# Kernel tuning notes

Hardware: AMD Instinct MI355X
Metric: run time of the kernel (lower is better)

## Reference

```python
import jax, jax.numpy as jnp
import numpy as np

SCALE = 1.0  # noise std from __init__


def setup_inputs() -> dict:
    key = jax.random.key(0)
    k1, k2, k3 = jax.random.split(key, 3)
    B, N, D, T = 32, 1024, 64, 2048
    data = jax.random.normal(k1, (B, N, D), dtype=jnp.float32)
    targets = jax.random.normal(k2, (B, N), dtype=jnp.float32)
    # W = task_pool.squeeze(-1).T, shape (n_dims, n_tasks)
    W = jax.random.normal(k3, (D, T), dtype=jnp.float32)
    return {"data": data, "targets": targets, "W": W}


def reference(data, targets, W):
    # data: (B, N, D), targets: (B, N), W: (D, T)
    dtype = data.dtype
    log_scale_sq = 2.0 * jnp.log(jnp.asarray(SCALE, dtype))
    # per-point per-task Gaussian log-likelihood terms
    XW = jnp.einsum('bnd,dt->bnt', data, W)                 # (B, N, T)
    diff = targets[..., None] - XW
    log_probs = -0.5 * ((diff / SCALE) ** 2 + log_scale_sq)  # (B, N, T)
    # exclusive prefix-sum over points: posterior at point i uses points < i.
    # At i=0 alpha=0 -> uniform weights -> W.mean(axis=1), matching the
    # original's explicit w_mean first step.
    cum = jnp.cumsum(log_probs, axis=1)
    alpha = jnp.concatenate([jnp.zeros_like(cum[:, :1]), cum[:, :-1]], axis=1)
    weights = jax.nn.softmax(alpha, axis=-1)                 # (B, N, T)
    w_mmse = jnp.einsum('bnt,dt->bnd', weights, W)           # (B, N, D)
    preds = jnp.einsum('bnd,bnd->bn', data, w_mmse)          # (B, N)
    return preds
```

## Files before the change

kernel.cpp:

```cpp
#include <hip/hip_runtime.h>
#include <hip/hip_bf16.h>
#include <math.h>

#define BB 32
#define NN 1024
#define DD 64
#define TT 2048
#define CHUNKS (TT / 256)
#define SEGS 16

typedef float f32x4 __attribute__((ext_vector_type(4)));
typedef unsigned short u16x4 __attribute__((ext_vector_type(4)));
using s16x8 = __attribute__((ext_vector_type(8))) short;

#define NLOG2E_HALF (-0.72134752044448169f)

__device__ __forceinline__ float exp2_fast(float x) {
    return __builtin_amdgcn_exp2f(x);
}

template<int CTRL>
__device__ __forceinline__ float dpp_mov_f(float v) {
    return __int_as_float(
        __builtin_amdgcn_mov_dpp(__float_as_int(v), CTRL, 0xF, 0xF, true));
}

template<int GB>
__device__ __forceinline__ float groupMax(float v) {
    v = fmaxf(v, dpp_mov_f<0x0B1>(v));
    v = fmaxf(v, dpp_mov_f<0x04E>(v));
    v = fmaxf(v, dpp_mov_f<0x141>(v));
    v = fmaxf(v, dpp_mov_f<0x140>(v));
    if constexpr (GB >= 5) v = fmaxf(v, __shfl_xor(v, 16));
    if constexpr (GB >= 6) v = fmaxf(v, __shfl_xor(v, 32));
    return v;
}

template<int GB>
__device__ __forceinline__ float groupSum(float v) {
    v += dpp_mov_f<0x0B1>(v);
    v += dpp_mov_f<0x04E>(v);
    v += dpp_mov_f<0x141>(v);
    v += dpp_mov_f<0x140>(v);
    if constexpr (GB >= 5) v += __shfl_xor(v, 16);
    if constexpr (GB >= 6) v += __shfl_xor(v, 32);
    return v;
}

__device__ __forceinline__ unsigned short bf16_rne(float x) {
    unsigned u = __float_as_uint(x);
    return (unsigned short)((u + 0x7FFFu + ((u >> 16) & 1u)) >> 16);
}
__device__ __forceinline__ void bf16_split(float x, unsigned short& hi,
                                           unsigned short& lo) {
    const unsigned short h = bf16_rne(x);
    const float xh = __uint_as_float(((unsigned)h) << 16);
    hi = h;
    lo = bf16_rne(x - xh);
}

__device__ __forceinline__ void loadW(const float* __restrict__ W, int col,
                                      f32x4* wv) {
#pragma unroll
    for (int i = 0; i < 16; ++i) {
        wv[i].x = W[(size_t)(4 * i + 0) * TT + col];
        wv[i].y = W[(size_t)(4 * i + 1) * TT + col];
        wv[i].z = W[(size_t)(4 * i + 2) * TT + col];
        wv[i].w = W[(size_t)(4 * i + 3) * TT + col];
    }
}

__device__ __forceinline__ float hsum(f32x4 s) {
    return (s.x + s.y) + (s.z + s.w);
}

__device__ __forceinline__ void dot4(const float* __restrict__ x0p,
                                     const f32x4* wv, float* xw) {
    const f32x4* xr0 = (const f32x4*)(x0p);
    const f32x4* xr1 = (const f32x4*)(x0p + DD);
    const f32x4* xr2 = (const f32x4*)(x0p + 2 * DD);
    const f32x4* xr3 = (const f32x4*)(x0p + 3 * DD);
    f32x4 s0 = {0.f, 0.f, 0.f, 0.f};
    f32x4 s1 = {0.f, 0.f, 0.f, 0.f};
    f32x4 s2 = {0.f, 0.f, 0.f, 0.f};
    f32x4 s3 = {0.f, 0.f, 0.f, 0.f};
#pragma unroll
    for (int i = 0; i < 16; ++i) {
        const f32x4 w = wv[i];
        s0 += xr0[i] * w;
        s1 += xr1[i] * w;
        s2 += xr2[i] * w;
        s3 += xr3[i] * w;
    }
    xw[0] = hsum(s0); xw[1] = hsum(s1); xw[2] = hsum(s2); xw[3] = hsum(s3);
}


__global__ __launch_bounds__(256)
void xsplit_kernel(const float* __restrict__ x,
                   unsigned short* __restrict__ xh,
                   unsigned short* __restrict__ xl)
{
    const int idx = (blockIdx.x * 256 + threadIdx.x) * 4;
    const f32x4 v = *(const f32x4*)(x + idx);
    u16x4 h, lo;
#pragma unroll
    for (int j = 0; j < 4; ++j) {
        unsigned short hh, ll;
        bf16_split(v[j], hh, ll);
        h[j] = hh; lo[j] = ll;
    }
    *(u16x4*)(xh + idx) = h;
    *(u16x4*)(xl + idx) = lo;
}

__global__ __launch_bounds__(256)
void wsplitT_kernel(const float* __restrict__ W,
                    unsigned short* __restrict__ whT,
                    unsigned short* __restrict__ wlT)
{
    const int idx = blockIdx.x * 256 + threadIdx.x;
    const int t = idx & (TT - 1);
    const int d = idx >> 11;
    unsigned short h, lo;
    bf16_split(W[(size_t)d * TT + t], h, lo);
    whT[(size_t)t * DD + d] = h;
    wlT[(size_t)t * DD + d] = lo;
}


__device__ __forceinline__ void loadB64_pre(const unsigned short* __restrict__ whT,
                                            const unsigned short* __restrict__ wlT,
                                            int colbase, int l,
                                            s16x8 bh[2][4], s16x8 bl[2][4]) {
    const int c0 = colbase + (l & 15);
    const int kb = (l >> 4) * 8;
#pragma unroll
    for (int ks = 0; ks < 2; ++ks)
#pragma unroll
        for (int nt = 0; nt < 4; ++nt) {
            const size_t off = (size_t)(c0 + nt * 16) * DD + ks * 32 + kb;
            bh[ks][nt] = *(const s16x8*)(whT + off);
            bl[ks][nt] = *(const s16x8*)(wlT + off);
        }
}

__device__ __forceinline__ void mfma_tile16_pre(const unsigned short* __restrict__ xh,
                                                const unsigned short* __restrict__ xl,
                                                int tile_n0, int l,
                                                const s16x8 bh[2][4],
                                                const s16x8 bl[2][4],
                                                f32x4 acc[4]) {
#pragma unroll
    for (int nt = 0; nt < 4; ++nt) acc[nt] = (f32x4){0.f, 0.f, 0.f, 0.f};
    const int row = tile_n0 + (l & 15);
#pragma unroll
    for (int ks = 0; ks < 2; ++ks) {
        const size_t off = (size_t)row * DD + ks * 32 + (l >> 4) * 8;
        const s16x8 ah = *(const s16x8*)(xh + off);
        const s16x8 al = *(const s16x8*)(xl + off);
#pragma unroll
        for (int nt = 0; nt < 4; ++nt) {
            acc[nt] = __builtin_amdgcn_mfma_f32_16x16x32_bf16(ah, bh[ks][nt], acc[nt], 0, 0, 0);
            acc[nt] = __builtin_amdgcn_mfma_f32_16x16x32_bf16(ah, bl[ks][nt], acc[nt], 0, 0, 0);
            acc[nt] = __builtin_amdgcn_mfma_f32_16x16x32_bf16(al, bh[ks][nt], acc[nt], 0, 0, 0);
        }
    }
}

template<int SEG>
__global__ __launch_bounds__(256)
void segsum_mfma_kernel(const unsigned short* __restrict__ xh,
                        const unsigned short* __restrict__ xl,
                        const unsigned short* __restrict__ whT,
                        const unsigned short* __restrict__ wlT,
                        const float* __restrict__ targets,
                        float* __restrict__ segsum)
{
    constexpr int NSEG = NN / SEG;
    __shared__ float ts[NSEG];

    const int blk   = blockIdx.x;
    const int s     = blk % SEG;
    const int rem   = blk / SEG;
    const int chunk = rem % CHUNKS;
    const int b     = rem / CHUNKS;
    const int tid   = threadIdx.x;
    const int wv    = tid >> 6;
    const int l     = tid & 63;

    const unsigned short* xbh = xh + (size_t)b * NN * DD;
    const unsigned short* xbl = xl + (size_t)b * NN * DD;
    const float* tb = targets + (size_t)b * NN;
    const int n0 = s * NSEG;

    if (tid < NSEG) ts[tid] = tb[n0 + tid];

    s16x8 bh[2][4], bl[2][4];
    loadB64_pre(whT, wlT, chunk * 256 + wv * 64, l, bh, bl);
    __syncthreads();

    float colacc[4] = {0.f, 0.f, 0.f, 0.f};

#pragma unroll 1
    for (int h = 0; h < NSEG / 16; ++h) {
        f32x4 acc[4];
        mfma_tile16_pre(xbh, xbl, n0 + h * 16, l, bh, bl, acc);
#pragma unroll
        for (int r = 0; r < 4; ++r) {
            const float tv = ts[h * 16 + (l >> 4) * 4 + r];
#pragma unroll
            for (int nt = 0; nt < 4; ++nt) {
                const float d = tv - acc[nt][r];
                colacc[nt] = fmaf(d * d, NLOG2E_HALF, colacc[nt]);
            }
        }
    }

#pragma unroll
    for (int nt = 0; nt < 4; ++nt) {
        colacc[nt] += __shfl_xor(colacc[nt], 16);
        colacc[nt] += __shfl_xor(colacc[nt], 32);
    }

    if (l < 16) {
        const size_t base = ((size_t)b * SEG + s) * TT + chunk * 256 + wv * 64 + l;
#pragma unroll
        for (int nt = 0; nt < 4; ++nt) segsum[base + nt * 16] = colacc[nt];
    }
}

template<int SEG, int GB>
__global__ __launch_bounds__(64)
void scan_mfma1_kernel(const unsigned short* __restrict__ xh,
                       const unsigned short* __restrict__ xl,
                       const unsigned short* __restrict__ whT,
                       const unsigned short* __restrict__ wlT,
                       const float* __restrict__ targets,
                       const float* __restrict__ segsum,
                       float* __restrict__ mP,
                       float* __restrict__ sP,
                       float* __restrict__ pP)
{
    constexpr int NSEG = NN / SEG;
    constexpr int MT   = 16;
    constexpr int CG   = TT / 64;
    constexpr int PPN  = TT >> GB;

    __shared__ __align__(16) float xw_tile[MT][68];

    const int blk = blockIdx.x;
    const int s   = blk % SEG;
    const int rem = blk / SEG;
    const int cg  = rem % CG;
    const int b   = rem / CG;
    const int l   = threadIdx.x;
    const int col = cg * 64 + l;

    const unsigned short* xbh = xh + (size_t)b * NN * DD;
    const unsigned short* xbl = xl + (size_t)b * NN * DD;
    const float* tb = targets + (size_t)b * NN;

    s16x8 bh[2][4], bl[2][4];
    loadB64_pre(whT, wlT, cg * 64, l, bh, bl);

    const int  k16    = col >> GB;
    const bool writer = (l & ((1 << GB) - 1)) == 0;
    const size_t base0 = (size_t)b * NN * PPN + k16;

    float alpha = 0.0f;
    if constexpr (SEG > 1) {
        for (int s2 = 0; s2 < s; ++s2)
            alpha += segsum[((size_t)b * SEG + s2) * TT + col];
    }

    const int n0 = s * NSEG;

#pragma unroll 1
    for (int h = 0; h < NSEG / MT; ++h) {
        f32x4 acc[4];
        mfma_tile16_pre(xbh, xbl, n0 + h * MT, l, bh, bl, acc);

#pragma unroll
        for (int nt = 0; nt < 4; ++nt)
#pragma unroll
            for (int r = 0; r < 4; ++r)
                xw_tile[(l >> 4) * 4 + r][nt * 16 + (l & 15)] = acc[nt][r];

#pragma unroll 1
        for (int q = 0; q < MT; q += 4) {
            const int n = n0 + h * MT + q;
            float xw[4];
#pragma unroll
            for (int j = 0; j < 4; ++j) xw[j] = xw_tile[q + j][l];

            float a[4];
            float al_ = alpha;
#pragma unroll
            for (int j = 0; j < 4; ++j) {
                a[j] = al_;
                const float d = tb[n + j] - xw[j];
                al_ = fmaf(d * d, NLOG2E_HALF, al_);
            }
            alpha = al_;

            float m[4], e[4], qv[4], sv[4], pv[4];
#pragma unroll
            for (int j = 0; j < 4; ++j) m[j] = groupMax<GB>(a[j]);
#pragma unroll
            for (int j = 0; j < 4; ++j) {
                e[j]  = exp2_fast(a[j] - m[j]);
                qv[j] = e[j] * xw[j];
            }
#pragma unroll
            for (int j = 0; j < 4; ++j) sv[j] = groupSum<GB>(e[j]);
#pragma unroll
            for (int j = 0; j < 4; ++j) pv[j] = groupSum<GB>(qv[j]);

            if (writer) {
                const size_t i0 = base0 + (size_t)n * PPN;
#pragma unroll
                for (int j = 0; j < 4; ++j) {
                    mP[i0 + (size_t)j * PPN] = m[j];
                    sP[i0 + (size_t)j * PPN] = sv[j];
                    pP[i0 + (size_t)j * PPN] = pv[j];
                }
            }
        }
    }
}

template<int SEG, int GB>
__global__ __launch_bounds__(256, 4)
void scan_kernel(const float* __restrict__ data,
                 const float* __restrict__ targets,
                 const float* __restrict__ W,
                 const float* __restrict__ segsum,
                 float* __restrict__ mP,
                 float* __restrict__ sP,
                 float* __restrict__ pP)
{
    constexpr int NSEG = NN / SEG;
    constexpr int PPN  = TT >> GB;
    const int blk   = blockIdx.x;
    const int s     = blk % SEG;
    const int rem   = blk / SEG;
    const int chunk = rem % CHUNKS;
    const int b     = rem / CHUNKS;
    const int tid   = threadIdx.x;
    const int lane  = tid & 63;
    const int col   = chunk * 256 + tid;

    f32x4 wv[16];
    loadW(W, col, wv);

    const float* xb = data + (size_t)b * NN * DD;
    const float* tb = targets + (size_t)b * NN;

    const int  k      = (chunk * 256 + (tid & ~((1 << GB) - 1))) >> GB;
    const bool writer = (lane & ((1 << GB) - 1)) == 0;
    const size_t base0 = (size_t)b * NN * PPN + k;

    float alpha = 0.0f;
    if constexpr (SEG > 1) {
        for (int s2 = 0; s2 < s; ++s2)
            alpha += segsum[((size_t)b * SEG + s2) * TT + col];
    }

    const int n0 = s * NSEG;
    for (int n = n0; n < n0 + NSEG; n += 4) {
        float xw[4];
        dot4(xb + (size_t)n * DD, wv, xw);
        float a[4];
        float al = alpha;
#pragma unroll
        for (int j = 0; j < 4; ++j) {
            a[j] = al;
            const float d = tb[n + j] - xw[j];
            al = fmaf(d * d, NLOG2E_HALF, al);
        }
        alpha = al;
        float m[4], e[4], qv[4], sv[4], pv[4];
#pragma unroll
        for (int j = 0; j < 4; ++j) m[j] = groupMax<GB>(a[j]);
#pragma unroll
        for (int j = 0; j < 4; ++j) {
            e[j]  = exp2_fast(a[j] - m[j]);
            qv[j] = e[j] * xw[j];
        }
#pragma unroll
        for (int j = 0; j < 4; ++j) sv[j] = groupSum<GB>(e[j]);
#pragma unroll
        for (int j = 0; j < 4; ++j) pv[j] = groupSum<GB>(qv[j]);
        if (writer) {
            const size_t i0 = base0 + (size_t)n * PPN;
#pragma unroll
            for (int j = 0; j < 4; ++j) {
                mP[i0 + (size_t)j * PPN] = m[j];
                sP[i0 + (size_t)j * PPN] = sv[j];
                pP[i0 + (size_t)j * PPN] = pv[j];
            }
        }
    }
}

template<int PPN>
__global__ __launch_bounds__(256)
void combine_kernel(const float* __restrict__ mP,
                    const float* __restrict__ sP,
                    const float* __restrict__ pP,
                    float* __restrict__ out)
{
    const int wgid = blockIdx.x * 4 + (threadIdx.x >> 6);
    const int lane = threadIdx.x & 63;
    const size_t base = (size_t)wgid * PPN;

    float m = -INFINITY, s = 0.0f, p = 0.0f;
    if constexpr (PPN >= 64) {
#pragma unroll
        for (int j = 0; j < PPN / 64; ++j) {
            const size_t idx = base + lane + j * 64;
            const float mk = mP[idx], sk = sP[idx], pk = pP[idx];
            const float M  = fmaxf(m, mk);
            const float e1 = exp2_fast(m - M), e2 = exp2_fast(mk - M);
            s = s * e1 + sk * e2;
            p = p * e1 + pk * e2;
            m = M;
        }
    } else {
        if (lane < PPN) {
            m = mP[base + lane]; s = sP[base + lane]; p = pP[base + lane];
        }
    }

#pragma unroll
    for (int off = 1; off < 64; off <<= 1) {
        const float mo = __shfl_xor(m, off);
        const float so = __shfl_xor(s, off);
        const float po = __shfl_xor(p, off);
        const float M  = fmaxf(m, mo);
        const float e1 = exp2_fast(m - M), e2 = exp2_fast(mo - M);
        s = s * e1 + so * e2;
        p = p * e1 + po * e2;
        m = M;
    }

    if (lane == 0) out[wgid] = p / s;
}

extern "C" void kernel_launch(void* const* d_in, const int* in_sizes, int n_in,
                              void* d_out, int out_size, void* d_ws, size_t ws_size,
                              hipStream_t stream)
{
    (void)in_sizes; (void)n_in; (void)out_size;
    const float* data    = (const float*)d_in[0];
    const float* targets = (const float*)d_in[1];
    const float* W       = (const float*)d_in[2];
    float* out = (float*)d_out;

    const size_t plane4 = (size_t)BB * NN * (TT >> 4);
    const size_t plane5 = (size_t)BB * NN * (TT >> 5);
    const size_t plane6 = (size_t)BB * NN * (TT >> 6);
    const size_t seg16  = (size_t)BB * SEGS * TT;
    const size_t xsplitF = (size_t)BB * NN * DD / 2;
    const size_t wsplitF = (size_t)TT * DD / 2;

    const int seg_grid  = BB * SEGS * CHUNKS;
    const int scan_grid = BB * (TT / 64) * SEGS;

    auto launch_pre = [&](size_t plane, auto scanTag) {
        float* mP = (float*)d_ws;
        float* sP = mP + plane;
        float* pP = sP + plane;
        float* sg = pP + plane;
        unsigned short* xh  = (unsigned short*)(sg + seg16);
        unsigned short* xl  = xh + (size_t)BB * NN * DD;
        unsigned short* whT = xl + (size_t)BB * NN * DD;
        unsigned short* wlT = whT + (size_t)TT * DD;

        xsplit_kernel<<<(BB * NN * DD) / (256 * 4), 256, 0, stream>>>(data, xh, xl);
        wsplitT_kernel<<<(TT * DD) / 256, 256, 0, stream>>>(W, whT, wlT);
        segsum_mfma_kernel<SEGS><<<seg_grid, 256, 0, stream>>>(xh, xl, whT, wlT, targets, sg);
        constexpr int GBv = decltype(scanTag)::value;
        scan_mfma1_kernel<SEGS, GBv><<<scan_grid, 64, 0, stream>>>(xh, xl, whT, wlT, targets, sg, mP, sP, pP);
        combine_kernel<(TT >> GBv)><<<(BB * NN) / 4, 256, 0, stream>>>(mP, sP, pP, out);
    };

    const size_t need4 = (3 * plane4 + seg16 + 2 * xsplitF + 2 * wsplitF) * sizeof(float);
    const size_t need5 = (3 * plane5 + seg16 + 2 * xsplitF + 2 * wsplitF) * sizeof(float);
    const size_t need6 = (3 * plane6 + seg16 + 2 * xsplitF + 2 * wsplitF) * sizeof(float);

    if (ws_size >= need4) {
        launch_pre(plane4, std::integral_constant<int, 4>{});
    } else if (ws_size >= need5) {
        launch_pre(plane5, std::integral_constant<int, 5>{});
    } else if (ws_size >= need6) {
        launch_pre(plane6, std::integral_constant<int, 6>{});
    } else {
        float* mP = (float*)d_ws;
        float* sP = mP + plane6;
        float* pP = sP + plane6;
        scan_kernel<1, 6><<<BB * CHUNKS, 256, 0, stream>>>(data, targets, W, nullptr, mP, sP, pP);
        combine_kernel<32><<<(BB * NN) / 4, 256, 0, stream>>>(mP, sP, pP, out);
    }
}
```

Baseline: 180.9 us.

## Merge split kernels into one launch and pack four scan waves per block

The separate x and W bf16-split kernels become a single launch whose blocks branch on block index, saving one kernel launch. The scan kernel moves from 64-thread blocks to 256-thread blocks, with four wavefronts each covering a different 64-column group and each using its own shared-memory tile slice. The intent is to reduce launch overhead and per-block scheduling cost and to improve occupancy packing. In exchange, each block needs four times the LDS, and the grid has a quarter as many blocks, which may change how work is balanced across CUs.

```diff
diff --git a/kernel.cpp b/kernel.cpp
--- a/kernel.cpp
+++ b/kernel.cpp
@@ -95,37 +95,38 @@
     xw[0] = hsum(s0); xw[1] = hsum(s1); xw[2] = hsum(s2); xw[3] = hsum(s3);
 }
 
-
+#define XB ((BB * NN * DD) / (256 * 4))
+#define WB ((TT * DD) / 256)
 __global__ __launch_bounds__(256)
-void xsplit_kernel(const float* __restrict__ x,
-                   unsigned short* __restrict__ xh,
-                   unsigned short* __restrict__ xl)
+void split_kernel(const float* __restrict__ x,
+                  const float* __restrict__ W,
+                  unsigned short* __restrict__ xh,
+                  unsigned short* __restrict__ xl,
+                  unsigned short* __restrict__ whT,
+                  unsigned short* __restrict__ wlT)
 {
-    const int idx = (blockIdx.x * 256 + threadIdx.x) * 4;
-    const f32x4 v = *(const f32x4*)(x + idx);
-    u16x4 h, lo;
-#pragma unroll
-    for (int j = 0; j < 4; ++j) {
-        unsigned short hh, ll;
-        bf16_split(v[j], hh, ll);
-        h[j] = hh; lo[j] = ll;
-    }
-    *(u16x4*)(xh + idx) = h;
-    *(u16x4*)(xl + idx) = lo;
-}
-
-__global__ __launch_bounds__(256)
-void wsplitT_kernel(const float* __restrict__ W,
-                    unsigned short* __restrict__ whT,
-                    unsigned short* __restrict__ wlT)
-{
-    const int idx = blockIdx.x * 256 + threadIdx.x;
-    const int t = idx & (TT - 1);
-    const int d = idx >> 11;
-    unsigned short h, lo;
-    bf16_split(W[(size_t)d * TT + t], h, lo);
-    whT[(size_t)t * DD + d] = h;
-    wlT[(size_t)t * DD + d] = lo;
+    const int gid = blockIdx.x;
+    if (gid < XB) {
+        const int idx = (gid * 256 + threadIdx.x) * 4;
+        const f32x4 v = *(const f32x4*)(x + idx);
+        u16x4 h, lo;
+#pragma unroll
+        for (int j = 0; j < 4; ++j) {
+            unsigned short hh, ll;
+            bf16_split(v[j], hh, ll);
+            h[j] = hh; lo[j] = ll;
+        }
+        *(u16x4*)(xh + idx) = h;
+        *(u16x4*)(xl + idx) = lo;
+    } else {
+        const int idx = (gid - XB) * 256 + threadIdx.x;
+        const int t = idx & (TT - 1);
+        const int d = idx >> 11;
+        unsigned short h, lo;
+        bf16_split(W[(size_t)d * TT + t], h, lo);
+        whT[(size_t)t * DD + d] = h;
+        wlT[(size_t)t * DD + d] = lo;
+    }
 }
 
 
@@ -231,8 +232,8 @@
 }
 
 template<int SEG, int GB>
-__global__ __launch_bounds__(64)
-void scan_mfma1_kernel(const unsigned short* __restrict__ xh,
+__global__ __launch_bounds__(256)
+void scan_mfma4_kernel(const unsigned short* __restrict__ xh,
                        const unsigned short* __restrict__ xl,
                        const unsigned short* __restrict__ whT,
                        const unsigned short* __restrict__ wlT,
@@ -244,17 +245,20 @@
 {
     constexpr int NSEG = NN / SEG;
     constexpr int MT   = 16;
-    constexpr int CG   = TT / 64;
+    constexpr int CGQ  = TT / 256;
     constexpr int PPN  = TT >> GB;
 
-    __shared__ __align__(16) float xw_tile[MT][68];
+    __shared__ __align__(16) float xw_tile[4][MT][68];
 
     const int blk = blockIdx.x;
     const int s   = blk % SEG;
     const int rem = blk / SEG;
-    const int cg  = rem % CG;
-    const int b   = rem / CG;
-    const int l   = threadIdx.x;
+    const int cgq = rem % CGQ;
+    const int b   = rem / CGQ;
+    const int tid = threadIdx.x;
+    const int wv  = tid >> 6;
+    const int l   = tid & 63;
+    const int cg  = cgq * 4 + wv;
     const int col = cg * 64 + l;
 
     const unsigned short* xbh = xh + (size_t)b * NN * DD;
@@ -285,14 +289,14 @@
         for (int nt = 0; nt < 4; ++nt)
 #pragma unroll
             for (int r = 0; r < 4; ++r)
-                xw_tile[(l >> 4) * 4 + r][nt * 16 + (l & 15)] = acc[nt][r];
+                xw_tile[wv][(l >> 4) * 4 + r][nt * 16 + (l & 15)] = acc[nt][r];
 
 #pragma unroll 1
         for (int q = 0; q < MT; q += 4) {
             const int n = n0 + h * MT + q;
             float xw[4];
 #pragma unroll
-            for (int j = 0; j < 4; ++j) xw[j] = xw_tile[q + j][l];
+            for (int j = 0; j < 4; ++j) xw[j] = xw_tile[wv][q + j][l];
 
             float a[4];
             float al_ = alpha;
@@ -466,9 +470,9 @@
     const size_t wsplitF = (size_t)TT * DD / 2;
 
     const int seg_grid  = BB * SEGS * CHUNKS;
-    const int scan_grid = BB * (TT / 64) * SEGS;
-
-    auto launch_pre = [&](size_t plane, auto scanTag) {
+    const int scan_grid = BB * (TT / 256) * SEGS;
+
+    auto launch_pre = [&](size_t plane, auto gbTag) {
         float* mP = (float*)d_ws;
         float* sP = mP + plane;
         float* pP = sP + plane;
@@ -478,11 +482,10 @@
         unsigned short* whT = xl + (size_t)BB * NN * DD;
         unsigned short* wlT = whT + (size_t)TT * DD;
 
-        xsplit_kernel<<<(BB * NN * DD) / (256 * 4), 256, 0, stream>>>(data, xh, xl);
-        wsplitT_kernel<<<(TT * DD) / 256, 256, 0, stream>>>(W, whT, wlT);
+        split_kernel<<<XB + WB, 256, 0, stream>>>(data, W, xh, xl, whT, wlT);
         segsum_mfma_kernel<SEGS><<<seg_grid, 256, 0, stream>>>(xh, xl, whT, wlT, targets, sg);
-        constexpr int GBv = decltype(scanTag)::value;
-        scan_mfma1_kernel<SEGS, GBv><<<scan_grid, 64, 0, stream>>>(xh, xl, whT, wlT, targets, sg, mP, sP, pP);
+        constexpr int GBv = decltype(gbTag)::value;
+        scan_mfma4_kernel<SEGS, GBv><<<scan_grid, 256, 0, stream>>>(xh, xl, whT, wlT, targets, sg, mP, sP, pP);
         combine_kernel<(TT >> GBv)><<<(BB * NN) / 4, 256, 0, stream>>>(mP, sP, pP, out);
     };
 
```

Measured after the change: 182.0 us. No clear change (+0.6%).

## Fuse bf16 split into segsum kernel and pair two segments per scan block

Applied to the files above, without the earlier changes.

Removes the separate x and W bf16 hi/lo split kernels: the segment-sum kernel now reads fp32 data and W directly, splits them in registers, and writes the split copies from designated blocks for the later scan kernel. The scan kernel now processes two segments per 64-thread block, interleaving the MFMA tile for the second segment with the softmax of the first to hide latency, which halves the grid. This cuts two launches and a full pass over the data, but adds redundant fp32 loads and split arithmetic in the segsum kernel. It also relies on the scan kernel seeing split data written by other blocks of the previous launch.

```diff
diff --git a/kernel.cpp b/kernel.cpp
--- a/kernel.cpp
+++ b/kernel.cpp
@@ -10,7 +10,6 @@
 #define SEGS 16
 
 typedef float f32x4 __attribute__((ext_vector_type(4)));
-typedef unsigned short u16x4 __attribute__((ext_vector_type(4)));
 using s16x8 = __attribute__((ext_vector_type(8))) short;
 
 #define NLOG2E_HALF (-0.72134752044448169f)
@@ -96,36 +95,67 @@
 }
 
 
-__global__ __launch_bounds__(256)
-void xsplit_kernel(const float* __restrict__ x,
-                   unsigned short* __restrict__ xh,
-                   unsigned short* __restrict__ xl)
-{
-    const int idx = (blockIdx.x * 256 + threadIdx.x) * 4;
-    const f32x4 v = *(const f32x4*)(x + idx);
-    u16x4 h, lo;
-#pragma unroll
-    for (int j = 0; j < 4; ++j) {
-        unsigned short hh, ll;
-        bf16_split(v[j], hh, ll);
-        h[j] = hh; lo[j] = ll;
-    }
-    *(u16x4*)(xh + idx) = h;
-    *(u16x4*)(xl + idx) = lo;
-}
-
-__global__ __launch_bounds__(256)
-void wsplitT_kernel(const float* __restrict__ W,
-                    unsigned short* __restrict__ whT,
-                    unsigned short* __restrict__ wlT)
-{
-    const int idx = blockIdx.x * 256 + threadIdx.x;
-    const int t = idx & (TT - 1);
-    const int d = idx >> 11;
-    unsigned short h, lo;
-    bf16_split(W[(size_t)d * TT + t], h, lo);
-    whT[(size_t)t * DD + d] = h;
-    wlT[(size_t)t * DD + d] = lo;
+__device__ __forceinline__ void loadB64_split(const float* __restrict__ W,
+                                              int colbase, int l,
+                                              s16x8 bh[2][4], s16x8 bl[2][4],
+                                              bool storeW,
+                                              unsigned short* __restrict__ whT,
+                                              unsigned short* __restrict__ wlT) {
+    const int c0  = colbase + (l & 15);
+    const int kb0 = (l >> 4) * 8;
+#pragma unroll
+    for (int ks = 0; ks < 2; ++ks)
+#pragma unroll
+        for (int nt = 0; nt < 4; ++nt) {
+            const int cw = c0 + nt * 16;
+#pragma unroll
+            for (int j = 0; j < 8; ++j) {
+                unsigned short h, lo_;
+                bf16_split(W[(size_t)(ks * 32 + kb0 + j) * TT + cw], h, lo_);
+                bh[ks][nt][j] = (short)h;
+                bl[ks][nt][j] = (short)lo_;
+            }
+            if (storeW) {
+                const size_t off = (size_t)cw * DD + ks * 32 + kb0;
+                *(s16x8*)(whT + off) = bh[ks][nt];
+                *(s16x8*)(wlT + off) = bl[ks][nt];
+            }
+        }
+}
+
+__device__ __forceinline__ void mfma_tile16_split(const float* __restrict__ xb,
+                                                  int tile_n0, int l,
+                                                  const s16x8 bh[2][4],
+                                                  const s16x8 bl[2][4],
+                                                  f32x4 acc[4],
+                                                  bool storeX,
+                                                  unsigned short* __restrict__ xhB,
+                                                  unsigned short* __restrict__ xlB) {
+#pragma unroll
+    for (int nt = 0; nt < 4; ++nt) acc[nt] = (f32x4){0.f, 0.f, 0.f, 0.f};
+    const int row = tile_n0 + (l & 15);
+#pragma unroll
+    for (int ks = 0; ks < 2; ++ks) {
+        const int kb = ks * 32 + (l >> 4) * 8;
+        s16x8 ah, al;
+#pragma unroll
+        for (int j = 0; j < 8; ++j) {
+            unsigned short hh, ll;
+            bf16_split(xb[(size_t)row * DD + kb + j], hh, ll);
+            ah[j] = (short)hh; al[j] = (short)ll;
+        }
+        if (storeX) {
+            const size_t off = (size_t)row * DD + kb;
+            *(s16x8*)(xhB + off) = ah;
+            *(s16x8*)(xlB + off) = al;
+        }
+#pragma unroll
+        for (int nt = 0; nt < 4; ++nt) {
+            acc[nt] = __builtin_amdgcn_mfma_f32_16x16x32_bf16(ah, bh[ks][nt], acc[nt], 0, 0, 0);
+            acc[nt] = __builtin_amdgcn_mfma_f32_16x16x32_bf16(ah, bl[ks][nt], acc[nt], 0, 0, 0);
+            acc[nt] = __builtin_amdgcn_mfma_f32_16x16x32_bf16(al, bh[ks][nt], acc[nt], 0, 0, 0);
+        }
+    }
 }
 
 
@@ -170,12 +200,14 @@
 
 template<int SEG>
 __global__ __launch_bounds__(256)
-void segsum_mfma_kernel(const unsigned short* __restrict__ xh,
-                        const unsigned short* __restrict__ xl,
-                        const unsigned short* __restrict__ whT,
-                        const unsigned short* __restrict__ wlT,
+void segsum_mfma_kernel(const float* __restrict__ data,
+                        const float* __restrict__ W,
                         const float* __restrict__ targets,
-                        float* __restrict__ segsum)
+                        float* __restrict__ segsum,
+                        unsigned short* __restrict__ xh,
+                        unsigned short* __restrict__ xl,
+                        unsigned short* __restrict__ whT,
+                        unsigned short* __restrict__ wlT)
 {
     constexpr int NSEG = NN / SEG;
     __shared__ float ts[NSEG];
@@ -189,15 +221,19 @@
     const int wv    = tid >> 6;
     const int l     = tid & 63;
 
-    const unsigned short* xbh = xh + (size_t)b * NN * DD;
-    const unsigned short* xbl = xl + (size_t)b * NN * DD;
+    const float* xb = data + (size_t)b * NN * DD;
     const float* tb = targets + (size_t)b * NN;
     const int n0 = s * NSEG;
 
     if (tid < NSEG) ts[tid] = tb[n0 + tid];
 
+    const bool storeW = (b == 0) && (s == 0);
+    const bool storeX = (chunk == 0) && (wv == 0);
+    unsigned short* xhB = xh + (size_t)b * NN * DD;
+    unsigned short* xlB = xl + (size_t)b * NN * DD;
+
     s16x8 bh[2][4], bl[2][4];
-    loadB64_pre(whT, wlT, chunk * 256 + wv * 64, l, bh, bl);
+    loadB64_split(W, chunk * 256 + wv * 64, l, bh, bl, storeW, whT, wlT);
     __syncthreads();
 
     float colacc[4] = {0.f, 0.f, 0.f, 0.f};
@@ -205,7 +241,7 @@
 #pragma unroll 1
     for (int h = 0; h < NSEG / 16; ++h) {
         f32x4 acc[4];
-        mfma_tile16_pre(xbh, xbl, n0 + h * 16, l, bh, bl, acc);
+        mfma_tile16_split(xb, n0 + h * 16, l, bh, bl, acc, storeX, xhB, xlB);
 #pragma unroll
         for (int r = 0; r < 4; ++r) {
             const float tv = ts[h * 16 + (l >> 4) * 4 + r];
@@ -232,7 +268,7 @@
 
 template<int SEG, int GB>
 __global__ __launch_bounds__(64)
-void scan_mfma1_kernel(const unsigned short* __restrict__ xh,
+void scan2_mfma_kernel(const unsigned short* __restrict__ xh,
                        const unsigned short* __restrict__ xl,
                        const unsigned short* __restrict__ whT,
                        const unsigned short* __restrict__ wlT,
@@ -244,16 +280,19 @@
 {
     constexpr int NSEG = NN / SEG;
     constexpr int MT   = 16;
+    constexpr int HALF = SEG / 2;
     constexpr int CG   = TT / 64;
     constexpr int PPN  = TT >> GB;
 
-    __shared__ __align__(16) float xw_tile[MT][68];
+    __shared__ __align__(16) float xwA[MT][68];
+    __shared__ __align__(16) float xwB[MT][68];
 
     const int blk = blockIdx.x;
-    const int s   = blk % SEG;
-    const int rem = blk / SEG;
+    const int sA  = blk % HALF;
+    const int rem = blk / HALF;
     const int cg  = rem % CG;
     const int b   = rem / CG;
+    const int sB  = sA + HALF;
     const int l   = threadIdx.x;
     const int col = cg * 64 + l;
 
@@ -268,31 +307,23 @@
     const bool writer = (l & ((1 << GB) - 1)) == 0;
     const size_t base0 = (size_t)b * NN * PPN + k16;
 
-    float alpha = 0.0f;
-    if constexpr (SEG > 1) {
-        for (int s2 = 0; s2 < s; ++s2)
-            alpha += segsum[((size_t)b * SEG + s2) * TT + col];
-    }
-
-    const int n0 = s * NSEG;
-
-#pragma unroll 1
-    for (int h = 0; h < NSEG / MT; ++h) {
-        f32x4 acc[4];
-        mfma_tile16_pre(xbh, xbl, n0 + h * MT, l, bh, bl, acc);
-
-#pragma unroll
-        for (int nt = 0; nt < 4; ++nt)
-#pragma unroll
-            for (int r = 0; r < 4; ++r)
-                xw_tile[(l >> 4) * 4 + r][nt * 16 + (l & 15)] = acc[nt][r];
-
+    float alphaA = 0.0f, alphaB = 0.0f;
+    for (int s2 = 0; s2 < sB; ++s2) {
+        const float v = segsum[((size_t)b * SEG + s2) * TT + col];
+        alphaB += v;
+        if (s2 < sA) alphaA += v;
+    }
+
+    const int nA0 = sA * NSEG;
+    const int nB0 = sB * NSEG;
+
+    auto softmax16 = [&](float& alpha, int nbase, const float (*tile)[68]) {
 #pragma unroll 1
         for (int q = 0; q < MT; q += 4) {
-            const int n = n0 + h * MT + q;
+            const int n = nbase + q;
             float xw[4];
 #pragma unroll
-            for (int j = 0; j < 4; ++j) xw[j] = xw_tile[q + j][l];
+            for (int j = 0; j < 4; ++j) xw[j] = tile[q + j][l];
 
             float a[4];
             float al_ = alpha;
@@ -327,6 +358,30 @@
                 }
             }
         }
+    };
+
+#pragma unroll 1
+    for (int h = 0; h < NSEG / MT; ++h) {
+        f32x4 accA[4];
+        mfma_tile16_pre(xbh, xbl, nA0 + h * MT, l, bh, bl, accA);
+#pragma unroll
+        for (int nt = 0; nt < 4; ++nt)
+#pragma unroll
+            for (int r = 0; r < 4; ++r)
+                xwA[(l >> 4) * 4 + r][nt * 16 + (l & 15)] = accA[nt][r];
+
+        f32x4 accB[4];
+        mfma_tile16_pre(xbh, xbl, nB0 + h * MT, l, bh, bl, accB);
+
+        softmax16(alphaA, nA0 + h * MT, xwA);
+
+#pragma unroll
+        for (int nt = 0; nt < 4; ++nt)
+#pragma unroll
+            for (int r = 0; r < 4; ++r)
+                xwB[(l >> 4) * 4 + r][nt * 16 + (l & 15)] = accB[nt][r];
+
+        softmax16(alphaB, nB0 + h * MT, xwB);
     }
 }
 
@@ -465,10 +520,10 @@
     const size_t xsplitF = (size_t)BB * NN * DD / 2;
     const size_t wsplitF = (size_t)TT * DD / 2;
 
-    const int seg_grid  = BB * SEGS * CHUNKS;
-    const int scan_grid = BB * (TT / 64) * SEGS;
-
-    auto launch_pre = [&](size_t plane, auto scanTag) {
+    const int seg_grid   = BB * SEGS * CHUNKS;
+    const int scan2_grid = BB * (TT / 64) * (SEGS / 2);
+
+    auto launch_pre = [&](size_t plane, auto gbTag) {
         float* mP = (float*)d_ws;
         float* sP = mP + plane;
         float* pP = sP + plane;
@@ -478,11 +533,11 @@
         unsigned short* whT = xl + (size_t)BB * NN * DD;
         unsigned short* wlT = whT + (size_t)TT * DD;
 
-        xsplit_kernel<<<(BB * NN * DD) / (256 * 4), 256, 0, stream>>>(data, xh, xl);
-        wsplitT_kernel<<<(TT * DD) / 256, 256, 0, stream>>>(W, whT, wlT);
-        segsum_mfma_kernel<SEGS><<<seg_grid, 256, 0, stream>>>(xh, xl, whT, wlT, targets, sg);
-        constexpr int GBv = decltype(scanTag)::value;
-        scan_mfma1_kernel<SEGS, GBv><<<scan_grid, 64, 0, stream>>>(xh, xl, whT, wlT, targets, sg, mP, sP, pP);
+        segsum_mfma_kernel<SEGS><<<seg_grid, 256, 0, stream>>>(
+            data, W, targets, sg, xh, xl, whT, wlT);
+        constexpr int GBv = decltype(gbTag)::value;
+        scan2_mfma_kernel<SEGS, GBv><<<scan2_grid, 64, 0, stream>>>(
+            xh, xl, whT, wlT, targets, sg, mP, sP, pP);
         combine_kernel<(TT >> GBv)><<<(BB * NN) / 4, 256, 0, stream>>>(mP, sP, pP, out);
     };
 
```

Result: faster. 173.1 us (-4.3%).
